# Kernel tuning notes

Measured on AMD Instinct MI355X. Metric: run time of the kernel, lower is better.

The kernel has to match this reference:

```python
import jax, jax.numpy as jnp
import numpy as np

N_GRAPHS = 32   # number of graphs (equal-size contiguous segments in `batch`)
SEG_LEN = 512   # nodes per graph
NUM_HEADS = 16
LN_EPS = 1e-5


def setup_inputs() -> dict:
    key = jax.random.key(0)
    ks = jax.random.split(key, 4)
    N = N_GRAPHS * SEG_LEN
    D = 1024
    x = jax.random.normal(ks[0], (N, D), dtype=jnp.float32)
    # contiguous equal-size graph segments (what per-graph batching produces)
    batch = jnp.repeat(jnp.arange(N_GRAPHS, dtype=jnp.int64), SEG_LEN)
    s = 1.0 / np.sqrt(D)
    w_in = jax.random.normal(ks[1], (3 * D, D), dtype=jnp.float32) * s
    b_in = jnp.zeros((3 * D,), dtype=jnp.float32)
    w_out = jax.random.normal(ks[2], (D, D), dtype=jnp.float32) * s
    b_out = jnp.zeros((D,), dtype=jnp.float32)
    gamma = jnp.ones((D,), dtype=jnp.float32)
    beta = jnp.zeros((D,), dtype=jnp.float32)
    return {"x": x, "batch": batch, "w_in": w_in, "b_in": b_in,
            "w_out": w_out, "b_out": b_out, "gamma": gamma, "beta": beta}


def _mha_blockdiag(x, w_in, b_in, w_out, b_out):
    # Packed per-graph self-attention: identical math to looping MHA over each
    # graph's node subset, but done in one dense batched attention.
    N, D = x.shape
    G, S, H = N_GRAPHS, SEG_LEN, NUM_HEADS
    dh = D // H
    qkv = x @ w_in.T + b_in                       # (N, 3D)
    qkv = qkv.reshape(G, S, 3, H, dh)
    q, k, v = qkv[:, :, 0], qkv[:, :, 1], qkv[:, :, 2]  # (G, S, H, dh)
    scale = 1.0 / jnp.sqrt(jnp.asarray(dh, x.dtype))
    scores = jnp.einsum('gqhd,gkhd->ghqk', q, k) * scale  # (G, H, S, S)
    probs = jax.nn.softmax(scores, axis=-1)
    ctx = jnp.einsum('ghqk,gkhd->gqhd', probs, v).reshape(N, D)
    return ctx @ w_out.T + b_out


def reference(x, batch, w_in, b_in, w_out, b_out, gamma, beta):
    attn_out = _mha_blockdiag(x, w_in, b_in, w_out, b_out)
    # dropout is identity in eval mode; residual + LayerNorm
    h = x + attn_out
    mu = jnp.mean(h, axis=-1, keepdims=True)
    var = jnp.var(h, axis=-1, keepdims=True)
    return (h - mu) * jax.lax.rsqrt(var + LN_EPS) * gamma + beta
```

## Files before the change

kernel.cpp:

```cpp
#include <hip/hip_runtime.h>
#include <hip/hip_bf16.h>
#include <math.h>

#define N_TOK  16384
#define DMODEL 1024
#define GRAPHS 32
#define SEGLEN 512
#define HEADS  16
#define DH     64
#define D3     3072
#define QK_LD  2048
#define KDIM   1024
#define NT_K   16

typedef __bf16 bf16;
typedef __attribute__((ext_vector_type(4))) __bf16 bf16x4;
typedef __attribute__((ext_vector_type(8))) __bf16 bf16x8;
typedef __attribute__((ext_vector_type(4))) float f32x4;

__global__ __launch_bounds__(256) void cvt_f32_bf16(const float* __restrict__ in,
                                                    bf16* __restrict__ out, int n4) {
    int i = blockIdx.x * blockDim.x + threadIdx.x;
    if (i < n4) {
        float4 v = ((const float4*)in)[i];
        bf16x4 o;
        o[0] = (bf16)v.x; o[1] = (bf16)v.y; o[2] = (bf16)v.z; o[3] = (bf16)v.w;
        ((bf16x4*)out)[i] = o;
    }
}

template<int EPI, int VSPLIT>
__global__ __launch_bounds__(256, 3) void gemm128(
    const bf16* __restrict__ A, const bf16* __restrict__ B,
    const float* __restrict__ bias, const float* __restrict__ resid,
    void* __restrict__ C, bf16* __restrict__ vT, int N, int nbn, int ldc)
{
    __shared__ bf16x8 smA[1024];
    __shared__ bf16x8 smB[1024];
    const int tid  = threadIdx.x;
    const int lane = tid & 63, w = tid >> 6;
    const int wr = w >> 1, wc = w & 1;
    const int l15 = lane & 15, l4 = lane >> 4;
    const int r7 = l15 & 7;

    const int nwg = (int)gridDim.x;
    const int bid = (int)blockIdx.x;
    const int sw  = (bid & 7) * (nwg >> 3) + (bid >> 3);
    const int bm0 = (sw / nbn) * 128, bn0 = (sw % nbn) * 128;

    const int srow = tid >> 3, skb = tid & 7;

    uint4 pa[4], pb[4];
    auto PF_LOAD = [&](int t) {
        const int k0 = t * 64;
        #pragma unroll
        for (int q = 0; q < 4; q++) {
            int row = q * 32 + srow;
            pa[q] = *(const uint4*)(A + (size_t)(bm0 + row) * KDIM + k0 + skb * 8);
            pb[q] = *(const uint4*)(B + (size_t)(bn0 + row) * KDIM + k0 + skb * 8);
        }
    };
    auto LDS_WRITE = [&]() {
        #pragma unroll
        for (int q = 0; q < 4; q++) {
            int row = q * 32 + srow;
            smA[row * 8 + (skb ^ (row & 7))] = __builtin_bit_cast(bf16x8, pa[q]);
            smB[row * 8 + (skb ^ (row & 7))] = __builtin_bit_cast(bf16x8, pb[q]);
        }
    };

    f32x4 acc[4][4] = {};

    PF_LOAD(0);
    LDS_WRITE();
    __syncthreads();

    #pragma unroll 1
    for (int t = 0; t < NT_K; ++t) {
        if (t + 1 < NT_K) PF_LOAD(t + 1);
        #pragma unroll
        for (int kp = 0; kp < 2; kp++) {
            const int slot = kp * 4 + l4;
            bf16x8 af[4], bfr[4];
            #pragma unroll
            for (int m = 0; m < 4; m++)
                af[m] = smA[(wr * 64 + m * 16 + l15) * 8 + (slot ^ r7)];
            #pragma unroll
            for (int n = 0; n < 4; n++)
                bfr[n] = smB[(wc * 64 + n * 16 + l15) * 8 + (slot ^ r7)];
            #pragma unroll
            for (int m = 0; m < 4; m++)
                #pragma unroll
                for (int n = 0; n < 4; n++)
                    acc[m][n] = __builtin_amdgcn_mfma_f32_16x16x32_bf16(af[m], bfr[n], acc[m][n], 0, 0, 0);
        }
        __syncthreads();
        if (t + 1 < NT_K) {
            LDS_WRITE();
            __syncthreads();
        }
    }

    #pragma unroll
    for (int m = 0; m < 4; m++) {
        #pragma unroll
        for (int n = 0; n < 4; n++) {
            const int col  = bn0 + wc * 64 + n * 16 + l15;
            const int row0 = bm0 + wr * 64 + m * 16 + l4 * 4;
            const float bv = bias[col];
            if (EPI == 1) {
                #pragma unroll
                for (int i = 0; i < 4; i++) {
                    float v = acc[m][n][i] + bv + resid[(size_t)(row0 + i) * N + col];
                    ((float*)C)[(size_t)(row0 + i) * N + col] = v;
                }
            } else if (VSPLIT && bn0 >= 2048) {
                const int cc = col - 2048;
                bf16x4 pk;
                #pragma unroll
                for (int i = 0; i < 4; i++) pk[i] = (bf16)(acc[m][n][i] + bv);
                *(bf16x4*)(vT + ((size_t)((row0 >> 9) * HEADS + (cc >> 6)) * DH + (cc & 63)) * SEGLEN
                               + (row0 & (SEGLEN - 1))) = pk;
            } else {
                const float sc = (VSPLIT && bn0 < 1024) ? 0.125f : 1.0f;
                #pragma unroll
                for (int i = 0; i < 4; i++)
                    ((bf16*)C)[(size_t)(row0 + i) * ldc + col] = (bf16)((acc[m][n][i] + bv) * sc);
            }
        }
    }
}

__global__ __launch_bounds__(256) void attn_kernel(
    const bf16* __restrict__ qkA, const bf16* __restrict__ vT, bf16* __restrict__ ctx)
{
    const int qt = blockIdx.x, h = blockIdx.y, g = blockIdx.z;
    __shared__ bf16x8 smQP[64 * 8];
    __shared__ bf16x8 smK[64 * 8];
    __shared__ bf16x8 smV[64 * 8];
    const int tid = threadIdx.x, lane = tid & 63, w = tid >> 6;
    const int l15 = lane & 15, l4 = lane >> 4;
    const int grow0 = g * SEGLEN;
    const size_t vbase = (size_t)(g * HEADS + h) * DH * SEGLEN;

    #pragma unroll
    for (int q = 0; q < 2; q++) {
        int c = tid + 256 * q, r = c >> 3, cb = c & 7;
        uint4 v = *(const uint4*)(qkA + (size_t)(grow0 + qt * 64 + r) * QK_LD + h * 64 + cb * 8);
        smQP[r * 8 + (cb ^ (r & 7))] = __builtin_bit_cast(bf16x8, v);
    }
    __syncthreads();

    bf16x8 qf[2];
    #pragma unroll
    for (int kp = 0; kp < 2; kp++) {
        int row = w * 16 + l15;
        qf[kp] = smQP[row * 8 + ((kp * 4 + l4) ^ (row & 7))];
    }

    f32x4 acc[4] = {};
    float mrow[4], lrow[4];
    #pragma unroll
    for (int i = 0; i < 4; i++) { mrow[i] = -INFINITY; lrow[i] = 0.f; }

    uint4 kr[2][2], vr[2][2];
    auto LOADT = [&](int t, int dst) {
        #pragma unroll
        for (int q = 0; q < 2; q++) {
            int c = tid + 256 * q, r = c >> 3, cb = c & 7;
            kr[dst][q] = *(const uint4*)(qkA + (size_t)(grow0 + t * 64 + r) * QK_LD + 1024 + h * 64 + cb * 8);
            vr[dst][q] = *(const uint4*)(vT + vbase + (size_t)r * SEGLEN + t * 64 + cb * 8);
        }
    };
    LOADT(0, 0);

    #pragma unroll
    for (int t = 0; t < 8; t++) {
        const int cur = t & 1, nxt = cur ^ 1;
        #pragma unroll
        for (int q = 0; q < 2; q++) {
            int c = tid + 256 * q, r = c >> 3, cb = c & 7;
            smK[r * 8 + (cb ^ (r & 7))] = __builtin_bit_cast(bf16x8, kr[cur][q]);
            smV[r * 8 + (cb ^ (r & 7))] = __builtin_bit_cast(bf16x8, vr[cur][q]);
        }
        if (t < 7) LOADT(t + 1, nxt);
        __syncthreads();

        f32x4 s[4] = {};
        #pragma unroll
        for (int kp = 0; kp < 2; kp++) {
            #pragma unroll
            for (int n = 0; n < 4; n++) {
                int row = n * 16 + l15;
                bf16x8 kf = smK[row * 8 + ((kp * 4 + l4) ^ (row & 7))];
                s[n] = __builtin_amdgcn_mfma_f32_16x16x32_bf16(qf[kp], kf, s[n], 0, 0, 0);
            }
        }
        float mx[4];
        #pragma unroll
        for (int i = 0; i < 4; i++) {
            float m0 = fmaxf(fmaxf(s[0][i], s[1][i]), fmaxf(s[2][i], s[3][i]));
            #pragma unroll
            for (int d = 1; d < 16; d <<= 1) m0 = fmaxf(m0, __shfl_xor(m0, d));
            mx[i] = m0;
        }
        int need = 0;
        #pragma unroll
        for (int i = 0; i < 4; i++) need |= (mx[i] > mrow[i] + 8.0f) ? 1 : 0;
        if (__any(need)) {
            #pragma unroll
            for (int i = 0; i < 4; i++) {
                float mn = fmaxf(mrow[i], mx[i]);
                float alpha = __expf(mrow[i] - mn);
                mrow[i] = mn;
                lrow[i] *= alpha;
                #pragma unroll
                for (int n = 0; n < 4; n++) acc[n][i] *= alpha;
            }
        }
        float rsum[4] = {0.f, 0.f, 0.f, 0.f};
        #pragma unroll
        for (int n = 0; n < 4; n++) {
            #pragma unroll
            for (int i = 0; i < 4; i++) {
                float p = __expf(s[n][i] - mrow[i]);
                rsum[i] += p;
                int prow = w * 16 + l4 * 4 + i;
                int pcol = n * 16 + l15;
                ((bf16*)smQP)[prow * 64 + (pcol ^ ((prow & 7) << 3))] = (bf16)p;
            }
        }
        #pragma unroll
        for (int i = 0; i < 4; i++) {
            #pragma unroll
            for (int d = 1; d < 16; d <<= 1) rsum[i] += __shfl_xor(rsum[i], d);
            lrow[i] += rsum[i];
        }
        #pragma unroll
        for (int kp = 0; kp < 2; kp++) {
            int prow = w * 16 + l15;
            bf16x8 pf = smQP[prow * 8 + ((kp * 4 + l4) ^ (prow & 7))];
            #pragma unroll
            for (int n = 0; n < 4; n++) {
                int vrow = n * 16 + l15;
                bf16x8 vf = smV[vrow * 8 + ((kp * 4 + l4) ^ (vrow & 7))];
                acc[n] = __builtin_amdgcn_mfma_f32_16x16x32_bf16(pf, vf, acc[n], 0, 0, 0);
            }
        }
        __syncthreads();
    }

    #pragma unroll
    for (int i = 0; i < 4; i++) {
        float inv = 1.f / lrow[i];
        int row = grow0 + qt * 64 + w * 16 + l4 * 4 + i;
        #pragma unroll
        for (int n = 0; n < 4; n++) {
            int col = h * 64 + n * 16 + l15;
            ctx[(size_t)row * DMODEL + col] = (bf16)(acc[n][i] * inv);
        }
    }
}

__global__ __launch_bounds__(256) void ln_kernel(
    const float* __restrict__ h, const float* __restrict__ gamma,
    const float* __restrict__ beta, float* __restrict__ out)
{
    const int row = blockIdx.x;
    float4 v = ((const float4*)(h + (size_t)row * DMODEL))[threadIdx.x];
    float s  = v.x + v.y + v.z + v.w;
    float ss = v.x * v.x + v.y * v.y + v.z * v.z + v.w * v.w;
    #pragma unroll
    for (int d = 1; d < 64; d <<= 1) { s += __shfl_xor(s, d); ss += __shfl_xor(ss, d); }
    __shared__ float red[8];
    int wv = threadIdx.x >> 6, lane = threadIdx.x & 63;
    if (lane == 0) { red[wv] = s; red[4 + wv] = ss; }
    __syncthreads();
    s  = red[0] + red[1] + red[2] + red[3];
    ss = red[4] + red[5] + red[6] + red[7];
    float mu  = s * (1.f / 1024.f);
    float var = ss * (1.f / 1024.f) - mu * mu;
    float rs  = rsqrtf(var + 1e-5f);
    float4 gv = ((const float4*)gamma)[threadIdx.x];
    float4 bv = ((const float4*)beta)[threadIdx.x];
    float4 o;
    o.x = (v.x - mu) * rs * gv.x + bv.x;
    o.y = (v.y - mu) * rs * gv.y + bv.y;
    o.z = (v.z - mu) * rs * gv.z + bv.z;
    o.w = (v.w - mu) * rs * gv.w + bv.w;
    ((float4*)(out + (size_t)row * DMODEL))[threadIdx.x] = o;
}

extern "C" void kernel_launch(void* const* d_in, const int* in_sizes, int n_in,
                              void* d_out, int out_size, void* d_ws, size_t ws_size,
                              hipStream_t stream) {
    const float* x     = (const float*)d_in[0];
    const float* w_in  = (const float*)d_in[2];
    const float* b_in  = (const float*)d_in[3];
    const float* w_out = (const float*)d_in[4];
    const float* b_out = (const float*)d_in[5];
    const float* gamma = (const float*)d_in[6];
    const float* beta  = (const float*)d_in[7];
    float* out = (float*)d_out;

    char* ws = (char*)d_ws;
    bf16*  xb   = (bf16*)ws;
    bf16*  wb   = (bf16*)(ws + 33554432);
    bf16*  wob  = (bf16*)(ws + 39845888);
    bf16*  qkA  = (bf16*)(ws + 41943040);
    bf16*  vT   = (bf16*)(ws + 109051904);
    bf16*  ctxb = xb;
    float* hbuf = (float*)qkA;

    cvt_f32_bf16<<<16384, 256, 0, stream>>>(x,     xb,  N_TOK * DMODEL / 4);
    cvt_f32_bf16<<<3072,  256, 0, stream>>>(w_in,  wb,  D3 * DMODEL / 4);
    cvt_f32_bf16<<<1024,  256, 0, stream>>>(w_out, wob, DMODEL * DMODEL / 4);

    gemm128<0, 1><<<3072, 256, 0, stream>>>(xb, wb, b_in, nullptr, qkA, vT,
                                            D3, 24, QK_LD);
    attn_kernel<<<dim3(8, 16, 32), 256, 0, stream>>>(qkA, vT, ctxb);

    gemm128<1, 0><<<1024, 256, 0, stream>>>(ctxb, wob, b_out, x, hbuf, nullptr,
                                            DMODEL, 8, DMODEL);
    ln_kernel<<<N_TOK, 256, 0, stream>>>(hbuf, gamma, beta, out);
}
```

Measured before the change: 338.4 us.

## Fuse x conversion into QKV GEMM, widen attention tiles, store residual in bf16

The QKV GEMM now reads fp32 x directly and converts it to bf16 while staging into shared memory, which removes the separate conversion kernel and its intermediate buffer. The attention kernel handles 128 query rows per block (two 16-row MFMA tiles per wave), so each K/V tile loaded into shared memory is reused for twice as many queries. The output GEMM writes the residual sum as bf16 and LayerNorm reads bf16, halving that round trip. GEMM occupancy hint rises to 4 and the block-to-tile mapping is reworked for locality. The pre-LayerNorm values lose precision from the bf16 storage, and the attention kernel uses more registers.

```diff
diff --git a/kernel.cpp b/kernel.cpp
--- a/kernel.cpp
+++ b/kernel.cpp
@@ -29,9 +29,9 @@
     }
 }
 
-template<int EPI, int VSPLIT>
-__global__ __launch_bounds__(256, 3) void gemm128(
-    const bf16* __restrict__ A, const bf16* __restrict__ B,
+template<int EPI, int VSPLIT, int CVT_A>
+__global__ __launch_bounds__(256, 4) void gemm128(
+    const void* __restrict__ Ap, const bf16* __restrict__ B,
     const float* __restrict__ bias, const float* __restrict__ resid,
     void* __restrict__ C, bf16* __restrict__ vT, int N, int nbn, int ldc)
 {
@@ -43,20 +43,29 @@
     const int l15 = lane & 15, l4 = lane >> 4;
     const int r7 = l15 & 7;
 
-    const int nwg = (int)gridDim.x;
-    const int bid = (int)blockIdx.x;
-    const int sw  = (bid & 7) * (nwg >> 3) + (bid >> 3);
-    const int bm0 = (sw / nbn) * 128, bn0 = (sw % nbn) * 128;
+    const int nwg  = (int)gridDim.x;
+    const int x    = (int)blockIdx.x & 7;
+    const int c    = (int)blockIdx.x >> 3;
+    const int nmt8 = (nwg >> 3) / nbn;
+    const int mt   = x * nmt8 + (c / (8 * nbn)) * 8 + (c & 7);
+    const int nt   = (c >> 3) % nbn;
+    const int bm0  = mt * 128, bn0 = nt * 128;
 
     const int srow = tid >> 3, skb = tid & 7;
 
-    uint4 pa[4], pb[4];
+    uint4 pa0[4], pa1[4], pb[4];
     auto PF_LOAD = [&](int t) {
         const int k0 = t * 64;
         #pragma unroll
         for (int q = 0; q < 4; q++) {
             int row = q * 32 + srow;
-            pa[q] = *(const uint4*)(A + (size_t)(bm0 + row) * KDIM + k0 + skb * 8);
+            if (CVT_A) {
+                const float* af = (const float*)Ap + (size_t)(bm0 + row) * KDIM + k0 + skb * 8;
+                pa0[q] = *(const uint4*)af;
+                pa1[q] = *(const uint4*)(af + 4);
+            } else {
+                pa0[q] = *(const uint4*)((const bf16*)Ap + (size_t)(bm0 + row) * KDIM + k0 + skb * 8);
+            }
             pb[q] = *(const uint4*)(B + (size_t)(bn0 + row) * KDIM + k0 + skb * 8);
         }
     };
@@ -64,7 +73,16 @@
         #pragma unroll
         for (int q = 0; q < 4; q++) {
             int row = q * 32 + srow;
-            smA[row * 8 + (skb ^ (row & 7))] = __builtin_bit_cast(bf16x8, pa[q]);
+            bf16x8 av;
+            if (CVT_A) {
+                float4 lo = __builtin_bit_cast(float4, pa0[q]);
+                float4 hi = __builtin_bit_cast(float4, pa1[q]);
+                av[0] = (bf16)lo.x; av[1] = (bf16)lo.y; av[2] = (bf16)lo.z; av[3] = (bf16)lo.w;
+                av[4] = (bf16)hi.x; av[5] = (bf16)hi.y; av[6] = (bf16)hi.z; av[7] = (bf16)hi.w;
+            } else {
+                av = __builtin_bit_cast(bf16x8, pa0[q]);
+            }
+            smA[row * 8 + (skb ^ (row & 7))] = av;
             smB[row * 8 + (skb ^ (row & 7))] = __builtin_bit_cast(bf16x8, pb[q]);
         }
     };
@@ -112,7 +130,7 @@
                 #pragma unroll
                 for (int i = 0; i < 4; i++) {
                     float v = acc[m][n][i] + bv + resid[(size_t)(row0 + i) * N + col];
-                    ((float*)C)[(size_t)(row0 + i) * N + col] = v;
+                    ((bf16*)C)[(size_t)(row0 + i) * ldc + col] = (bf16)v;
                 }
             } else if (VSPLIT && bn0 >= 2048) {
                 const int cc = col - 2048;
@@ -135,33 +153,38 @@
     const bf16* __restrict__ qkA, const bf16* __restrict__ vT, bf16* __restrict__ ctx)
 {
     const int qt = blockIdx.x, h = blockIdx.y, g = blockIdx.z;
-    __shared__ bf16x8 smQP[64 * 8];
+    __shared__ bf16x8 smQP[128 * 8];
     __shared__ bf16x8 smK[64 * 8];
     __shared__ bf16x8 smV[64 * 8];
     const int tid = threadIdx.x, lane = tid & 63, w = tid >> 6;
     const int l15 = lane & 15, l4 = lane >> 4;
-    const int grow0 = g * SEGLEN;
+    const int r7 = l15 & 7;
+    const int grow0 = g * SEGLEN, qbase = qt * 128;
     const size_t vbase = (size_t)(g * HEADS + h) * DH * SEGLEN;
 
     #pragma unroll
-    for (int q = 0; q < 2; q++) {
+    for (int q = 0; q < 4; q++) {
         int c = tid + 256 * q, r = c >> 3, cb = c & 7;
-        uint4 v = *(const uint4*)(qkA + (size_t)(grow0 + qt * 64 + r) * QK_LD + h * 64 + cb * 8);
+        uint4 v = *(const uint4*)(qkA + (size_t)(grow0 + qbase + r) * QK_LD + h * 64 + cb * 8);
         smQP[r * 8 + (cb ^ (r & 7))] = __builtin_bit_cast(bf16x8, v);
     }
     __syncthreads();
 
-    bf16x8 qf[2];
-    #pragma unroll
-    for (int kp = 0; kp < 2; kp++) {
-        int row = w * 16 + l15;
-        qf[kp] = smQP[row * 8 + ((kp * 4 + l4) ^ (row & 7))];
-    }
-
-    f32x4 acc[4] = {};
-    float mrow[4], lrow[4];
-    #pragma unroll
-    for (int i = 0; i < 4; i++) { mrow[i] = -INFINITY; lrow[i] = 0.f; }
+    bf16x8 qf[2][2];
+    #pragma unroll
+    for (int m = 0; m < 2; m++)
+        #pragma unroll
+        for (int kp = 0; kp < 2; kp++) {
+            int row = w * 32 + m * 16 + l15;
+            qf[m][kp] = smQP[row * 8 + ((kp * 4 + l4) ^ (row & 7))];
+        }
+
+    f32x4 acc[2][4] = {};
+    float mrow[2][4], lrow[2][4];
+    #pragma unroll
+    for (int m = 0; m < 2; m++)
+        #pragma unroll
+        for (int i = 0; i < 4; i++) { mrow[m][i] = -INFINITY; lrow[m][i] = 0.f; }
 
     uint4 kr[2][2], vr[2][2];
     auto LOADT = [&](int t, int dst) {
@@ -176,100 +199,112 @@
 
     #pragma unroll
     for (int t = 0; t < 8; t++) {
-        const int cur = t & 1, nxt = cur ^ 1;
+        const int cur = t & 1;
         #pragma unroll
         for (int q = 0; q < 2; q++) {
             int c = tid + 256 * q, r = c >> 3, cb = c & 7;
             smK[r * 8 + (cb ^ (r & 7))] = __builtin_bit_cast(bf16x8, kr[cur][q]);
             smV[r * 8 + (cb ^ (r & 7))] = __builtin_bit_cast(bf16x8, vr[cur][q]);
         }
-        if (t < 7) LOADT(t + 1, nxt);
+        if (t < 7) LOADT(t + 1, cur ^ 1);
         __syncthreads();
 
-        f32x4 s[4] = {};
+        f32x4 s[2][4] = {};
         #pragma unroll
         for (int kp = 0; kp < 2; kp++) {
             #pragma unroll
             for (int n = 0; n < 4; n++) {
-                int row = n * 16 + l15;
-                bf16x8 kf = smK[row * 8 + ((kp * 4 + l4) ^ (row & 7))];
-                s[n] = __builtin_amdgcn_mfma_f32_16x16x32_bf16(qf[kp], kf, s[n], 0, 0, 0);
-            }
-        }
-        float mx[4];
+                bf16x8 kf = smK[(n * 16 + l15) * 8 + ((kp * 4 + l4) ^ r7)];
+                #pragma unroll
+                for (int m = 0; m < 2; m++)
+                    s[m][n] = __builtin_amdgcn_mfma_f32_16x16x32_bf16(qf[m][kp], kf, s[m][n], 0, 0, 0);
+            }
+        }
+        float mx[2][4];
+        int need = 0;
+        #pragma unroll
+        for (int m = 0; m < 2; m++)
+            #pragma unroll
+            for (int i = 0; i < 4; i++) {
+                float m0 = fmaxf(fmaxf(s[m][0][i], s[m][1][i]), fmaxf(s[m][2][i], s[m][3][i]));
+                #pragma unroll
+                for (int d = 1; d < 16; d <<= 1) m0 = fmaxf(m0, __shfl_xor(m0, d));
+                mx[m][i] = m0;
+                need |= (m0 > mrow[m][i] + 8.0f) ? 1 : 0;
+            }
+        if (__any(need)) {
+            #pragma unroll
+            for (int m = 0; m < 2; m++)
+                #pragma unroll
+                for (int i = 0; i < 4; i++) {
+                    float mn = fmaxf(mrow[m][i], mx[m][i]);
+                    float alpha = __expf(mrow[m][i] - mn);
+                    mrow[m][i] = mn;
+                    lrow[m][i] *= alpha;
+                    #pragma unroll
+                    for (int n = 0; n < 4; n++) acc[m][n][i] *= alpha;
+                }
+        }
+        float rsum[2][4] = {};
+        #pragma unroll
+        for (int m = 0; m < 2; m++)
+            #pragma unroll
+            for (int n = 0; n < 4; n++)
+                #pragma unroll
+                for (int i = 0; i < 4; i++) {
+                    float p = __expf(s[m][n][i] - mrow[m][i]);
+                    rsum[m][i] += p;
+                    int prow = w * 32 + m * 16 + l4 * 4 + i;
+                    ((bf16*)smQP)[prow * 64 + ((n * 16 + l15) ^ ((prow & 7) << 3))] = (bf16)p;
+                }
+        #pragma unroll
+        for (int m = 0; m < 2; m++)
+            #pragma unroll
+            for (int i = 0; i < 4; i++) {
+                #pragma unroll
+                for (int d = 1; d < 16; d <<= 1) rsum[m][i] += __shfl_xor(rsum[m][i], d);
+                lrow[m][i] += rsum[m][i];
+            }
+        #pragma unroll
+        for (int kp = 0; kp < 2; kp++) {
+            bf16x8 pf[2];
+            #pragma unroll
+            for (int m = 0; m < 2; m++)
+                pf[m] = smQP[(w * 32 + m * 16 + l15) * 8 + ((kp * 4 + l4) ^ r7)];
+            #pragma unroll
+            for (int n = 0; n < 4; n++) {
+                bf16x8 vf = smV[(n * 16 + l15) * 8 + ((kp * 4 + l4) ^ r7)];
+                #pragma unroll
+                for (int m = 0; m < 2; m++)
+                    acc[m][n] = __builtin_amdgcn_mfma_f32_16x16x32_bf16(pf[m], vf, acc[m][n], 0, 0, 0);
+            }
+        }
+        __syncthreads();
+    }
+
+    #pragma unroll
+    for (int m = 0; m < 2; m++)
         #pragma unroll
         for (int i = 0; i < 4; i++) {
-            float m0 = fmaxf(fmaxf(s[0][i], s[1][i]), fmaxf(s[2][i], s[3][i]));
-            #pragma unroll
-            for (int d = 1; d < 16; d <<= 1) m0 = fmaxf(m0, __shfl_xor(m0, d));
-            mx[i] = m0;
-        }
-        int need = 0;
-        #pragma unroll
-        for (int i = 0; i < 4; i++) need |= (mx[i] > mrow[i] + 8.0f) ? 1 : 0;
-        if (__any(need)) {
-            #pragma unroll
-            for (int i = 0; i < 4; i++) {
-                float mn = fmaxf(mrow[i], mx[i]);
-                float alpha = __expf(mrow[i] - mn);
-                mrow[i] = mn;
-                lrow[i] *= alpha;
-                #pragma unroll
-                for (int n = 0; n < 4; n++) acc[n][i] *= alpha;
-            }
-        }
-        float rsum[4] = {0.f, 0.f, 0.f, 0.f};
-        #pragma unroll
-        for (int n = 0; n < 4; n++) {
-            #pragma unroll
-            for (int i = 0; i < 4; i++) {
-                float p = __expf(s[n][i] - mrow[i]);
-                rsum[i] += p;
-                int prow = w * 16 + l4 * 4 + i;
-                int pcol = n * 16 + l15;
-                ((bf16*)smQP)[prow * 64 + (pcol ^ ((prow & 7) << 3))] = (bf16)p;
-            }
-        }
-        #pragma unroll
-        for (int i = 0; i < 4; i++) {
-            #pragma unroll
-            for (int d = 1; d < 16; d <<= 1) rsum[i] += __shfl_xor(rsum[i], d);
-            lrow[i] += rsum[i];
-        }
-        #pragma unroll
-        for (int kp = 0; kp < 2; kp++) {
-            int prow = w * 16 + l15;
-            bf16x8 pf = smQP[prow * 8 + ((kp * 4 + l4) ^ (prow & 7))];
+            float inv = 1.f / lrow[m][i];
+            int row = grow0 + qbase + w * 32 + m * 16 + l4 * 4 + i;
             #pragma unroll
             for (int n = 0; n < 4; n++) {
-                int vrow = n * 16 + l15;
-                bf16x8 vf = smV[vrow * 8 + ((kp * 4 + l4) ^ (vrow & 7))];
-                acc[n] = __builtin_amdgcn_mfma_f32_16x16x32_bf16(pf, vf, acc[n], 0, 0, 0);
-            }
-        }
-        __syncthreads();
-    }
-
-    #pragma unroll
-    for (int i = 0; i < 4; i++) {
-        float inv = 1.f / lrow[i];
-        int row = grow0 + qt * 64 + w * 16 + l4 * 4 + i;
-        #pragma unroll
-        for (int n = 0; n < 4; n++) {
-            int col = h * 64 + n * 16 + l15;
-            ctx[(size_t)row * DMODEL + col] = (bf16)(acc[n][i] * inv);
-        }
-    }
+                int col = h * 64 + n * 16 + l15;
+                ctx[(size_t)row * DMODEL + col] = (bf16)(acc[m][n][i] * inv);
+            }
+        }
 }
 
 __global__ __launch_bounds__(256) void ln_kernel(
-    const float* __restrict__ h, const float* __restrict__ gamma,
+    const bf16* __restrict__ h, const float* __restrict__ gamma,
     const float* __restrict__ beta, float* __restrict__ out)
 {
     const int row = blockIdx.x;
-    float4 v = ((const float4*)(h + (size_t)row * DMODEL))[threadIdx.x];
-    float s  = v.x + v.y + v.z + v.w;
-    float ss = v.x * v.x + v.y * v.y + v.z * v.z + v.w * v.w;
+    bf16x4 hv = ((const bf16x4*)(h + (size_t)row * DMODEL))[threadIdx.x];
+    float v0 = (float)hv[0], v1 = (float)hv[1], v2 = (float)hv[2], v3 = (float)hv[3];
+    float s  = v0 + v1 + v2 + v3;
+    float ss = v0 * v0 + v1 * v1 + v2 * v2 + v3 * v3;
     #pragma unroll
     for (int d = 1; d < 64; d <<= 1) { s += __shfl_xor(s, d); ss += __shfl_xor(ss, d); }
     __shared__ float red[8];
@@ -284,10 +319,10 @@
     float4 gv = ((const float4*)gamma)[threadIdx.x];
     float4 bv = ((const float4*)beta)[threadIdx.x];
     float4 o;
-    o.x = (v.x - mu) * rs * gv.x + bv.x;
-    o.y = (v.y - mu) * rs * gv.y + bv.y;
-    o.z = (v.z - mu) * rs * gv.z + bv.z;
-    o.w = (v.w - mu) * rs * gv.w + bv.w;
+    o.x = (v0 - mu) * rs * gv.x + bv.x;
+    o.y = (v1 - mu) * rs * gv.y + bv.y;
+    o.z = (v2 - mu) * rs * gv.z + bv.z;
+    o.w = (v3 - mu) * rs * gv.w + bv.w;
     ((float4*)(out + (size_t)row * DMODEL))[threadIdx.x] = o;
 }
 
@@ -304,23 +339,21 @@
     float* out = (float*)d_out;
 
     char* ws = (char*)d_ws;
-    bf16*  xb   = (bf16*)ws;
+    bf16*  ctxb = (bf16*)ws;
     bf16*  wb   = (bf16*)(ws + 33554432);
     bf16*  wob  = (bf16*)(ws + 39845888);
     bf16*  qkA  = (bf16*)(ws + 41943040);
     bf16*  vT   = (bf16*)(ws + 109051904);
-    bf16*  ctxb = xb;
-    float* hbuf = (float*)qkA;
-
-    cvt_f32_bf16<<<16384, 256, 0, stream>>>(x,     xb,  N_TOK * DMODEL / 4);
-    cvt_f32_bf16<<<3072,  256, 0, stream>>>(w_in,  wb,  D3 * DMODEL / 4);
-    cvt_f32_bf16<<<1024,  256, 0, stream>>>(w_out, wob, DMODEL * DMODEL / 4);
-
-    gemm128<0, 1><<<3072, 256, 0, stream>>>(xb, wb, b_in, nullptr, qkA, vT,
-                                            D3, 24, QK_LD);
-    attn_kernel<<<dim3(8, 16, 32), 256, 0, stream>>>(qkA, vT, ctxb);
-
-    gemm128<1, 0><<<1024, 256, 0, stream>>>(ctxb, wob, b_out, x, hbuf, nullptr,
-                                            DMODEL, 8, DMODEL);
+    bf16*  hbuf = qkA;
+
+    cvt_f32_bf16<<<3072, 256, 0, stream>>>(w_in,  wb,  D3 * DMODEL / 4);
+    cvt_f32_bf16<<<1024, 256, 0, stream>>>(w_out, wob, DMODEL * DMODEL / 4);
+
+    gemm128<0, 1, 1><<<3072, 256, 0, stream>>>(x, wb, b_in, nullptr, qkA, vT,
+                                               D3, 24, QK_LD);
+    attn_kernel<<<dim3(4, 16, 32), 256, 0, stream>>>(qkA, vT, ctxb);
+
+    gemm128<1, 0, 0><<<1024, 256, 0, stream>>>(ctxb, wob, b_out, x, hbuf, nullptr,
+                                               DMODEL, 8, DMODEL);
     ln_kernel<<<N_TOK, 256, 0, stream>>>(hbuf, gamma, beta, out);
 }
```

Result: slower. 712.0 us (+110.4%).
